# Performance work log

Hardware: AMD Instinct MI355X
Metric: run time of the kernel (lower is better)

Reference implementation:

```python
import jax, jax.numpy as jnp
import numpy as np
import math

MEMORY_SIZE = 50000
FEATURE_SIZE = 4096  # = 64*8*8
HASH_SIZE = 128
B, C, H, W = 64, 64, 8, 8


def setup_inputs() -> dict:
    key = jax.random.key(0)
    k1, k2, k3, k4 = jax.random.split(key, 4)
    stdv = 1.0 / math.sqrt(FEATURE_SIZE)
    feature = jax.random.normal(k1, (B, C, H, W), dtype=jnp.float32)
    memory = jax.random.uniform(k2, (MEMORY_SIZE, FEATURE_SIZE), minval=-stdv, maxval=stdv, dtype=jnp.float32)
    # nn.Linear default init: U(-1/sqrt(fan_in), 1/sqrt(fan_in))
    hash_W = jax.random.uniform(k3, (HASH_SIZE, FEATURE_SIZE), minval=-stdv, maxval=stdv, dtype=jnp.float32)
    hash_b = jax.random.uniform(k4, (HASH_SIZE,), minval=-stdv, maxval=stdv, dtype=jnp.float32)
    return {"feature": feature, "memory": memory, "hash_W": hash_W, "hash_b": hash_b}


def _binarize(x, hash_W, hash_b):
    # 0.5 * (sign(Linear(x) - 0.5) + 1)  -> values in {0, 1} (0.5 only on measure-zero ties)
    return 0.5 * (jnp.sign(x @ hash_W.T + hash_b - 0.5) + 1.0)


def reference(feature, memory, hash_W, hash_b):
    b, c, h, w = feature.shape
    flat = feature.reshape(b, c * h * w)                      # [B, F]
    hm = _binarize(memory, hash_W, hash_b)                    # [M, 128]
    hf = _binarize(flat, hash_W, hash_b)                      # [B, 128]
    # For binary a,b: |a - b| = a + b - 2ab, so the L1 (Hamming) distance is a GEMM:
    HD = (hf.sum(-1, keepdims=True) + hm.sum(-1)[None, :]
          - 2.0 * (hf @ hm.T))                                # [B, M]
    idx = jnp.argmin(HD, axis=1)                              # [B]
    recon = memory[idx]                                       # gather nearest memory rows
    return recon.reshape(b, c, h, w)
```

## Files before the change

kernel.cpp:

```cpp
#include <hip/hip_runtime.h>
#include <hip/hip_bf16.h>
#include <stdint.h>
#include <stddef.h>

typedef __attribute__((ext_vector_type(8))) short s8v;
typedef __attribute__((ext_vector_type(4))) float f32x4;
typedef __attribute__((ext_vector_type(4))) uint32_t u32x4;
typedef __attribute__((ext_vector_type(4))) unsigned short u16x4;

#define KDIM 4096
#define NH   128
#define MMEM 50000
#define BFEAT 64
#define NGRP 3125
#define NBLK 256
#define NGMAX 13
#define NSEG 8

static __device__ __forceinline__ unsigned short f2bf(float f) {
  union { float f; uint32_t u; } c; c.f = f;
  uint32_t u = c.u;
  return (unsigned short)((u + 0x7FFFu + ((u >> 16) & 1u)) >> 16);
}

static __device__ __forceinline__ short f2bfs(float f) {
  __hip_bfloat16 h = __float2bfloat16(f);
  short s;
  __builtin_memcpy(&s, &h, sizeof(s));
  return s;
}

__global__ __launch_bounds__(256) void prep_kernel(
    const float* __restrict__ W, unsigned short* __restrict__ Wb,
    const float* __restrict__ flat, const float* __restrict__ hb,
    unsigned char* __restrict__ hf_bytes, unsigned int* __restrict__ keys) {
  const int bid = blockIdx.x;
  const int t   = threadIdx.x;
  if (bid < 512) {
    if (bid == 0 && t < BFEAT) keys[t] = 0xFFFFFFFFu;
    int i = bid * 256 + t;
    f32x4 v = reinterpret_cast<const f32x4*>(W)[i];
    u16x4 o;
    o[0] = f2bf(v[0]); o[1] = f2bf(v[1]); o[2] = f2bf(v[2]); o[3] = f2bf(v[3]);
    reinterpret_cast<u16x4*>(Wb)[i] = o;
  } else {
    int did  = (bid - 512) * 4 + (t >> 6);
    int n = did & 127, b = did >> 7;
    int lane = t & 63;
    const f32x4* fa = reinterpret_cast<const f32x4*>(flat + (size_t)b * KDIM);
    const f32x4* wa = reinterpret_cast<const f32x4*>(W + (size_t)n * KDIM);
    float s = 0.f;
#pragma unroll 4
    for (int q = 0; q < 16; ++q) {
      f32x4 x = fa[lane + 64 * q], y = wa[lane + 64 * q];
      s += x[0] * y[0] + x[1] * y[1] + x[2] * y[2] + x[3] * y[3];
    }
    for (int o = 32; o; o >>= 1) s += __shfl_down(s, o, 64);
    if (lane == 0) hf_bytes[b * NH + n] = (s + hb[n] - 0.5f) > 0.f ? 1 : 0;
  }
}


__global__ __launch_bounds__(512, 2) void hash_bits_kernel(
    const float* __restrict__ A,
    const unsigned short* __restrict__ Wb,
    const float* __restrict__ hb,
    uint32_t* __restrict__ out_bits) {
  __shared__ short Abuf[2][NGMAX * 16 * 64];
  __shared__ unsigned short smb[NGMAX * 16][8];

  const int t    = threadIdx.x;
  const int lane = t & 63;
  const int w    = t >> 6;
  const int l15  = lane & 15;
  const int kq   = lane >> 4;
  const int b    = blockIdx.x;
  const int koff = b & 63;
  const int g0   = (b * NGRP) >> 8;
  const int NG   = (((b + 1) * NGRP) >> 8) - g0;
  const int row0 = g0 * 16;

  const float* srcA[4];
  int ldsoff[4];
#pragma unroll
  for (int p = 0; p < 4; ++p) {
    int P  = t + 512 * p;
    int g  = P >> 7;
    int q  = P & 127;
    int r  = q >> 3;
    int kg = q & 7;
    srcA[p]   = A + (size_t)(row0 + g * 16 + r) * KDIM + kg * 8;
    ldsoff[p] = (g * 16 + r) * 64 + ((kg ^ (r & 7)) << 3);
  }
  const bool v3 = (t + 1536) < NG * 128;

  const unsigned short* pb = Wb + (size_t)(16 * w + l15) * KDIM + kq * 8;
  const float hbv = hb[16 * w + l15];

  f32x4 acc[NGMAX];
#pragma unroll
  for (int g = 0; g < NGMAX; ++g) acc[g] = (f32x4){0.f, 0.f, 0.f, 0.f};

  f32x4 aR[4][2];
  s8v bA0, bA1, bB0, bB1;

#define PCH(S) (((S) + koff) & 63)

#define LOADA(CH) do {                                                        \
  const f32x4* q0 = reinterpret_cast<const f32x4*>(srcA[0] + (CH) * 64);      \
  aR[0][0] = q0[0]; aR[0][1] = q0[1];                                         \
  const f32x4* q1 = reinterpret_cast<const f32x4*>(srcA[1] + (CH) * 64);      \
  aR[1][0] = q1[0]; aR[1][1] = q1[1];                                         \
  const f32x4* q2 = reinterpret_cast<const f32x4*>(srcA[2] + (CH) * 64);      \
  aR[2][0] = q2[0]; aR[2][1] = q2[1];                                         \
  if (v3) {                                                                   \
    const f32x4* q3 = reinterpret_cast<const f32x4*>(srcA[3] + (CH) * 64);    \
    aR[3][0] = q3[0]; aR[3][1] = q3[1];                                       \
  }                                                                           \
} while (0)

#define CVTW1(P, BUFW) do {                                                   \
  s8v av;                                                                     \
  av[0] = f2bfs(aR[P][0][0]); av[1] = f2bfs(aR[P][0][1]);                     \
  av[2] = f2bfs(aR[P][0][2]); av[3] = f2bfs(aR[P][0][3]);                     \
  av[4] = f2bfs(aR[P][1][0]); av[5] = f2bfs(aR[P][1][1]);                     \
  av[6] = f2bfs(aR[P][1][2]); av[7] = f2bfs(aR[P][1][3]);                     \
  *reinterpret_cast<s8v*>(&(BUFW)[ldsoff[P]]) = av;                           \
} while (0)

#define CVTWRITE(BUFW) do {                                                   \
  CVTW1(0, BUFW); CVTW1(1, BUFW); CVTW1(2, BUFW);                             \
  if (v3) CVTW1(3, BUFW);                                                     \
} while (0)

#define LOADB(CH, B0, B1) do {                                                \
  B0 = *reinterpret_cast<const s8v*>(pb + (CH) * 64);                         \
  B1 = *reinterpret_cast<const s8v*>(pb + (CH) * 64 + 32);                    \
} while (0)

#define COMPUTE(BUFR, B0, B1) do {                                            \
  _Pragma("unroll")                                                           \
  for (int g = 0; g < NGMAX; ++g) {                                           \
    const s8v af = *reinterpret_cast<const s8v*>(                             \
        &(BUFR)[(g * 16 + l15) * 64 + ((kq ^ (l15 & 7)) << 3)]);              \
    acc[g] = __builtin_amdgcn_mfma_f32_16x16x32_bf16(af, B0, acc[g], 0, 0, 0);\
  }                                                                           \
  _Pragma("unroll")                                                           \
  for (int g = 0; g < NGMAX; ++g) {                                           \
    const s8v af = *reinterpret_cast<const s8v*>(                             \
        &(BUFR)[(g * 16 + l15) * 64 + (((4 + kq) ^ (l15 & 7)) << 3)]);        \
    acc[g] = __builtin_amdgcn_mfma_f32_16x16x32_bf16(af, B1, acc[g], 0, 0, 0);\
  }                                                                           \
} while (0)

#define BARRIER() do {                                                        \
  asm volatile("s_waitcnt lgkmcnt(0)" ::: "memory");                          \
  __builtin_amdgcn_s_barrier();                                               \
  __builtin_amdgcn_sched_barrier(0);                                          \
} while (0)

#define STEP(S, BUFR, BUFW, B0, B1) do {                                      \
  BARRIER();                                                                  \
  COMPUTE(BUFR, B0, B1);                                                      \
  if ((S) + 1 < 64) CVTWRITE(BUFW);                                           \
  if ((S) + 2 < 64) { LOADA(PCH((S) + 2)); LOADB(PCH((S) + 2), B0, B1); }     \
} while (0)

  LOADA(PCH(0));
  CVTWRITE(Abuf[0]);
  LOADA(PCH(1));
  LOADB(PCH(0), bA0, bA1);
  LOADB(PCH(1), bB0, bB1);

  for (int s2 = 0; s2 < 64; s2 += 2) {
    STEP(s2 + 0, Abuf[0], Abuf[1], bA0, bA1);
    STEP(s2 + 1, Abuf[1], Abuf[0], bB0, bB1);
  }

#pragma unroll
  for (int g = 0; g < NGMAX; ++g) {
#pragma unroll
    for (int r = 0; r < 4; ++r) {
      uint64_t mask = __ballot(acc[g][r] + hbv - 0.5f > 0.f);
      if (l15 == r)
        smb[g * 16 + (lane >> 4) * 4 + r][w] =
            (unsigned short)((mask >> (16 * (lane >> 4))) & 0xFFFFu);
    }
  }
  __syncthreads();
  const int rows = NG * 16;
  if (t < rows) {
    uint32_t w0 = (uint32_t)smb[t][0] | ((uint32_t)smb[t][1] << 16);
    uint32_t w1 = (uint32_t)smb[t][2] | ((uint32_t)smb[t][3] << 16);
    uint32_t w2 = (uint32_t)smb[t][4] | ((uint32_t)smb[t][5] << 16);
    uint32_t w3 = (uint32_t)smb[t][6] | ((uint32_t)smb[t][7] << 16);
    reinterpret_cast<u32x4*>(out_bits)[row0 + t] = (u32x4){w0, w1, w2, w3};
  }
}

__global__ __launch_bounds__(256) void argmin_part_kernel(
    const uint32_t* __restrict__ hm_bits, const unsigned char* __restrict__ hf_bytes,
    int M, unsigned int* __restrict__ keys) {
  __shared__ uint32_t red[256];
  const int b   = blockIdx.x & (BFEAT - 1);
  const int seg = blockIdx.x / BFEAT;
  const int span = (M + NSEG - 1) / NSEG;
  const int m0 = seg * span;
  int m1 = m0 + span; if (m1 > M) m1 = M;
  const int t = threadIdx.x;
  uint64_t hf0 = 0, hf1 = 0;
  const unsigned char* hfb = hf_bytes + b * NH;
  for (int c = 0; c < 64; ++c) {
    hf0 |= (uint64_t)(hfb[c] & 1u) << c;
    hf1 |= (uint64_t)(hfb[c + 64] & 1u) << c;
  }
  int hfsum = __popcll(hf0) + __popcll(hf1);
  uint32_t best = 0xFFFFFFFFu;
  for (int m = m0 + t; m < m1; m += 256) {
    u32x4 pv = reinterpret_cast<const u32x4*>(hm_bits)[m];
    uint64_t h0 = (uint64_t)pv[0] | ((uint64_t)pv[1] << 32);
    uint64_t h1 = (uint64_t)pv[2] | ((uint64_t)pv[3] << 32);
    int hmsum = __popcll(h0) + __popcll(h1);
    int dot   = __popcll(h0 & hf0) + __popcll(h1 & hf1);
    int hd    = hfsum + hmsum - 2 * dot;
    uint32_t key = ((uint32_t)hd << 16) | (uint32_t)m;
    best = best < key ? best : key;
  }
  red[t] = best;
  __syncthreads();
  for (int s = 128; s > 0; s >>= 1) {
    if (t < s) red[t] = red[t] < red[t + s] ? red[t] : red[t + s];
    __syncthreads();
  }
  if (t == 0) atomicMin(&keys[b], red[0]);
}

__global__ __launch_bounds__(256) void gather_kernel(
    const float* __restrict__ memory, const unsigned int* __restrict__ keys,
    float* __restrict__ out) {
  int b = blockIdx.x;
  int t = threadIdx.x;
  int m = (int)(keys[b] & 0xFFFFu);
  const f32x4* src = reinterpret_cast<const f32x4*>(memory + (size_t)m * KDIM);
  f32x4* dst = reinterpret_cast<f32x4*>(out + (size_t)b * KDIM);
#pragma unroll
  for (int c = 0; c < 4; ++c) dst[t + 256 * c] = src[t + 256 * c];
}

extern "C" void kernel_launch(void* const* d_in, const int* in_sizes, int n_in,
                              void* d_out, int out_size, void* d_ws, size_t ws_size,
                              hipStream_t stream) {
  const float* feature = (const float*)d_in[0];
  const float* memory  = (const float*)d_in[1];
  const float* hash_W  = (const float*)d_in[2];
  const float* hash_b  = (const float*)d_in[3];
  float* out = (float*)d_out;

  char* ws = (char*)d_ws;
  unsigned short* Wb       = (unsigned short*)ws;
  uint32_t*       hm_bits  = (uint32_t*)(ws + 1048576);
  unsigned char*  hf_bytes = (unsigned char*)(ws + 1048576 + 800000);
  unsigned int*   keys     = (unsigned int*)(ws + 1048576 + 800000 + 8192);

  prep_kernel<<<2560, 256, 0, stream>>>(hash_W, Wb, feature, hash_b, hf_bytes, keys);
  hash_bits_kernel<<<NBLK, 512, 0, stream>>>(memory, Wb, hash_b, hm_bits);
  argmin_part_kernel<<<BFEAT * NSEG, 256, 0, stream>>>(hm_bits, hf_bytes, MMEM, keys);
  gather_kernel<<<BFEAT, 256, 0, stream>>>(memory, keys, out);
}
```

Measured before the change: 175.2 us.

## Double hash-bits grid to 512 blocks and fuse argmin with gather

The hash-bits GEMM now runs on 512 blocks with fewer row groups each (NGMAX 7, occupancy hint raised to 4 blocks per CU), so more CUs are busy and register pressure drops. Row indices are clamped so tail blocks cannot read past the memory array. The segmented argmin with atomicMin and the separate gather kernel become one kernel: a 512-thread block per query scans all memory rows and then copies the winning row itself. This removes a launch and the key initialisation, but each query's scan now runs in a single block instead of eight.

```diff
diff --git a/kernel.cpp b/kernel.cpp
--- a/kernel.cpp
+++ b/kernel.cpp
@@ -13,9 +13,9 @@
 #define MMEM 50000
 #define BFEAT 64
 #define NGRP 3125
-#define NBLK 256
-#define NGMAX 13
-#define NSEG 8
+#define NBLK 512
+#define NGMAX 7
+#define MLANES 512
 
 static __device__ __forceinline__ unsigned short f2bf(float f) {
   union { float f; uint32_t u; } c; c.f = f;
@@ -33,11 +33,10 @@
 __global__ __launch_bounds__(256) void prep_kernel(
     const float* __restrict__ W, unsigned short* __restrict__ Wb,
     const float* __restrict__ flat, const float* __restrict__ hb,
-    unsigned char* __restrict__ hf_bytes, unsigned int* __restrict__ keys) {
+    unsigned char* __restrict__ hf_bytes) {
   const int bid = blockIdx.x;
   const int t   = threadIdx.x;
   if (bid < 512) {
-    if (bid == 0 && t < BFEAT) keys[t] = 0xFFFFFFFFu;
     int i = bid * 256 + t;
     f32x4 v = reinterpret_cast<const f32x4*>(W)[i];
     u16x4 o;
@@ -61,7 +60,7 @@
 }
 
 
-__global__ __launch_bounds__(512, 2) void hash_bits_kernel(
+__global__ __launch_bounds__(512, 4) void hash_bits_kernel(
     const float* __restrict__ A,
     const unsigned short* __restrict__ Wb,
     const float* __restrict__ hb,
@@ -76,23 +75,25 @@
   const int kq   = lane >> 4;
   const int b    = blockIdx.x;
   const int koff = b & 63;
-  const int g0   = (b * NGRP) >> 8;
-  const int NG   = (((b + 1) * NGRP) >> 8) - g0;
+  const int g0   = (b * NGRP) >> 9;
+  const int NG   = (((b + 1) * NGRP) >> 9) - g0;
   const int row0 = g0 * 16;
 
-  const float* srcA[4];
-  int ldsoff[4];
-#pragma unroll
-  for (int p = 0; p < 4; ++p) {
+  const float* srcA[2];
+  int ldsoff[2];
+#pragma unroll
+  for (int p = 0; p < 2; ++p) {
     int P  = t + 512 * p;
     int g  = P >> 7;
     int q  = P & 127;
     int r  = q >> 3;
     int kg = q & 7;
-    srcA[p]   = A + (size_t)(row0 + g * 16 + r) * KDIM + kg * 8;
+    int row = row0 + g * 16 + r;
+    if (row > MMEM - 1) row = MMEM - 1;
+    srcA[p]   = A + (size_t)row * KDIM + kg * 8;
     ldsoff[p] = (g * 16 + r) * 64 + ((kg ^ (r & 7)) << 3);
   }
-  const bool v3 = (t + 1536) < NG * 128;
+  const bool v1 = (t + 512) < NG * 128;
 
   const unsigned short* pb = Wb + (size_t)(16 * w + l15) * KDIM + kq * 8;
   const float hbv = hb[16 * w + l15];
@@ -101,7 +102,7 @@
 #pragma unroll
   for (int g = 0; g < NGMAX; ++g) acc[g] = (f32x4){0.f, 0.f, 0.f, 0.f};
 
-  f32x4 aR[4][2];
+  f32x4 aR[2][2];
   s8v bA0, bA1, bB0, bB1;
 
 #define PCH(S) (((S) + koff) & 63)
@@ -109,13 +110,9 @@
 #define LOADA(CH) do {                                                        \
   const f32x4* q0 = reinterpret_cast<const f32x4*>(srcA[0] + (CH) * 64);      \
   aR[0][0] = q0[0]; aR[0][1] = q0[1];                                         \
-  const f32x4* q1 = reinterpret_cast<const f32x4*>(srcA[1] + (CH) * 64);      \
-  aR[1][0] = q1[0]; aR[1][1] = q1[1];                                         \
-  const f32x4* q2 = reinterpret_cast<const f32x4*>(srcA[2] + (CH) * 64);      \
-  aR[2][0] = q2[0]; aR[2][1] = q2[1];                                         \
-  if (v3) {                                                                   \
-    const f32x4* q3 = reinterpret_cast<const f32x4*>(srcA[3] + (CH) * 64);    \
-    aR[3][0] = q3[0]; aR[3][1] = q3[1];                                       \
+  if (v1) {                                                                   \
+    const f32x4* q1 = reinterpret_cast<const f32x4*>(srcA[1] + (CH) * 64);    \
+    aR[1][0] = q1[0]; aR[1][1] = q1[1];                                       \
   }                                                                           \
 } while (0)
 
@@ -129,8 +126,8 @@
 } while (0)
 
 #define CVTWRITE(BUFW) do {                                                   \
-  CVTW1(0, BUFW); CVTW1(1, BUFW); CVTW1(2, BUFW);                             \
-  if (v3) CVTW1(3, BUFW);                                                     \
+  CVTW1(0, BUFW);                                                             \
+  if (v1) CVTW1(1, BUFW);                                                     \
 } while (0)
 
 #define LOADB(CH, B0, B1) do {                                                \
@@ -198,15 +195,11 @@
   }
 }
 
-__global__ __launch_bounds__(256) void argmin_part_kernel(
+__global__ __launch_bounds__(512) void argmin_gather_kernel(
     const uint32_t* __restrict__ hm_bits, const unsigned char* __restrict__ hf_bytes,
-    int M, unsigned int* __restrict__ keys) {
-  __shared__ uint32_t red[256];
-  const int b   = blockIdx.x & (BFEAT - 1);
-  const int seg = blockIdx.x / BFEAT;
-  const int span = (M + NSEG - 1) / NSEG;
-  const int m0 = seg * span;
-  int m1 = m0 + span; if (m1 > M) m1 = M;
+    const float* __restrict__ memory, float* __restrict__ out) {
+  __shared__ uint32_t red[MLANES];
+  const int b = blockIdx.x;
   const int t = threadIdx.x;
   uint64_t hf0 = 0, hf1 = 0;
   const unsigned char* hfb = hf_bytes + b * NH;
@@ -216,7 +209,7 @@
   }
   int hfsum = __popcll(hf0) + __popcll(hf1);
   uint32_t best = 0xFFFFFFFFu;
-  for (int m = m0 + t; m < m1; m += 256) {
+  for (int m = t; m < MMEM; m += MLANES) {
     u32x4 pv = reinterpret_cast<const u32x4*>(hm_bits)[m];
     uint64_t h0 = (uint64_t)pv[0] | ((uint64_t)pv[1] << 32);
     uint64_t h1 = (uint64_t)pv[2] | ((uint64_t)pv[3] << 32);
@@ -228,23 +221,15 @@
   }
   red[t] = best;
   __syncthreads();
-  for (int s = 128; s > 0; s >>= 1) {
+  for (int s = MLANES / 2; s > 0; s >>= 1) {
     if (t < s) red[t] = red[t] < red[t + s] ? red[t] : red[t + s];
     __syncthreads();
   }
-  if (t == 0) atomicMin(&keys[b], red[0]);
-}
-
-__global__ __launch_bounds__(256) void gather_kernel(
-    const float* __restrict__ memory, const unsigned int* __restrict__ keys,
-    float* __restrict__ out) {
-  int b = blockIdx.x;
-  int t = threadIdx.x;
-  int m = (int)(keys[b] & 0xFFFFu);
+  const int m = (int)(red[0] & 0xFFFFu);
   const f32x4* src = reinterpret_cast<const f32x4*>(memory + (size_t)m * KDIM);
   f32x4* dst = reinterpret_cast<f32x4*>(out + (size_t)b * KDIM);
-#pragma unroll
-  for (int c = 0; c < 4; ++c) dst[t + 256 * c] = src[t + 256 * c];
+  dst[t]       = src[t];
+  dst[t + 512] = src[t + 512];
 }
 
 extern "C" void kernel_launch(void* const* d_in, const int* in_sizes, int n_in,
@@ -260,10 +245,8 @@
   unsigned short* Wb       = (unsigned short*)ws;
   uint32_t*       hm_bits  = (uint32_t*)(ws + 1048576);
   unsigned char*  hf_bytes = (unsigned char*)(ws + 1048576 + 800000);
-  unsigned int*   keys     = (unsigned int*)(ws + 1048576 + 800000 + 8192);
-
-  prep_kernel<<<2560, 256, 0, stream>>>(hash_W, Wb, feature, hash_b, hf_bytes, keys);
+
+  prep_kernel<<<2560, 256, 0, stream>>>(hash_W, Wb, feature, hash_b, hf_bytes);
   hash_bits_kernel<<<NBLK, 512, 0, stream>>>(memory, Wb, hash_b, hm_bits);
-  argmin_part_kernel<<<BFEAT * NSEG, 256, 0, stream>>>(hm_bits, hf_bytes, MMEM, keys);
-  gather_kernel<<<BFEAT, 256, 0, stream>>>(memory, keys, out);
-}
+  argmin_gather_kernel<<<BFEAT, 512, 0, stream>>>(hm_bits, hf_bytes, memory, out);
+}
```

Result: slower. 199.6 us (+13.9%).

## Fuse prep, argmin and gather kernels; convert hash weights in-loop

Applied to the files above, without the earlier changes.

Drops the separate prep kernel. The hash weights are now loaded as fp32 and converted to bf16 inside the MFMA loop. The feature hash, the argmin over all memory rows and the gather are merged into one kernel with one block per batch item, so there is no atomic and no key initialisation. This cuts the launch count from four to two and removes intermediate global buffers. In exchange, the hash weight loads are twice as large, the conversions run inside the hot loop, and the argmin now runs on only 64 blocks, each scanning all 50000 rows and recomputing 128 dot products per block.

```diff
diff --git a/kernel.cpp b/kernel.cpp
--- a/kernel.cpp
+++ b/kernel.cpp
@@ -6,7 +6,6 @@
 typedef __attribute__((ext_vector_type(8))) short s8v;
 typedef __attribute__((ext_vector_type(4))) float f32x4;
 typedef __attribute__((ext_vector_type(4))) uint32_t u32x4;
-typedef __attribute__((ext_vector_type(4))) unsigned short u16x4;
 
 #define KDIM 4096
 #define NH   128
@@ -15,13 +14,7 @@
 #define NGRP 3125
 #define NBLK 256
 #define NGMAX 13
-#define NSEG 8
-
-static __device__ __forceinline__ unsigned short f2bf(float f) {
-  union { float f; uint32_t u; } c; c.f = f;
-  uint32_t u = c.u;
-  return (unsigned short)((u + 0x7FFFu + ((u >> 16) & 1u)) >> 16);
-}
+#define MLANES 512
 
 static __device__ __forceinline__ short f2bfs(float f) {
   __hip_bfloat16 h = __float2bfloat16(f);
@@ -30,40 +23,10 @@
   return s;
 }
 
-__global__ __launch_bounds__(256) void prep_kernel(
-    const float* __restrict__ W, unsigned short* __restrict__ Wb,
-    const float* __restrict__ flat, const float* __restrict__ hb,
-    unsigned char* __restrict__ hf_bytes, unsigned int* __restrict__ keys) {
-  const int bid = blockIdx.x;
-  const int t   = threadIdx.x;
-  if (bid < 512) {
-    if (bid == 0 && t < BFEAT) keys[t] = 0xFFFFFFFFu;
-    int i = bid * 256 + t;
-    f32x4 v = reinterpret_cast<const f32x4*>(W)[i];
-    u16x4 o;
-    o[0] = f2bf(v[0]); o[1] = f2bf(v[1]); o[2] = f2bf(v[2]); o[3] = f2bf(v[3]);
-    reinterpret_cast<u16x4*>(Wb)[i] = o;
-  } else {
-    int did  = (bid - 512) * 4 + (t >> 6);
-    int n = did & 127, b = did >> 7;
-    int lane = t & 63;
-    const f32x4* fa = reinterpret_cast<const f32x4*>(flat + (size_t)b * KDIM);
-    const f32x4* wa = reinterpret_cast<const f32x4*>(W + (size_t)n * KDIM);
-    float s = 0.f;
-#pragma unroll 4
-    for (int q = 0; q < 16; ++q) {
-      f32x4 x = fa[lane + 64 * q], y = wa[lane + 64 * q];
-      s += x[0] * y[0] + x[1] * y[1] + x[2] * y[2] + x[3] * y[3];
-    }
-    for (int o = 32; o; o >>= 1) s += __shfl_down(s, o, 64);
-    if (lane == 0) hf_bytes[b * NH + n] = (s + hb[n] - 0.5f) > 0.f ? 1 : 0;
-  }
-}
-
 
 __global__ __launch_bounds__(512, 2) void hash_bits_kernel(
     const float* __restrict__ A,
-    const unsigned short* __restrict__ Wb,
+    const float* __restrict__ Wf,
     const float* __restrict__ hb,
     uint32_t* __restrict__ out_bits) {
   __shared__ short Abuf[2][NGMAX * 16 * 64];
@@ -94,7 +57,7 @@
   }
   const bool v3 = (t + 1536) < NG * 128;
 
-  const unsigned short* pb = Wb + (size_t)(16 * w + l15) * KDIM + kq * 8;
+  const float* pbf = Wf + (size_t)(16 * w + l15) * KDIM + kq * 8;
   const float hbv = hb[16 * w + l15];
 
   f32x4 acc[NGMAX];
@@ -102,7 +65,7 @@
   for (int g = 0; g < NGMAX; ++g) acc[g] = (f32x4){0.f, 0.f, 0.f, 0.f};
 
   f32x4 aR[4][2];
-  s8v bA0, bA1, bB0, bB1;
+  f32x4 bA[4], bB[4];
 
 #define PCH(S) (((S) + koff) & 63)
 
@@ -133,23 +96,34 @@
   if (v3) CVTW1(3, BUFW);                                                     \
 } while (0)
 
-#define LOADB(CH, B0, B1) do {                                                \
-  B0 = *reinterpret_cast<const s8v*>(pb + (CH) * 64);                         \
-  B1 = *reinterpret_cast<const s8v*>(pb + (CH) * 64 + 32);                    \
-} while (0)
-
-#define COMPUTE(BUFR, B0, B1) do {                                            \
+#define LOADB(CH, SET) do {                                                   \
+  const f32x4* qb0 = reinterpret_cast<const f32x4*>(pbf + (CH) * 64);         \
+  SET[0] = qb0[0]; SET[1] = qb0[1];                                           \
+  const f32x4* qb1 = reinterpret_cast<const f32x4*>(pbf + (CH) * 64 + 32);    \
+  SET[2] = qb1[0]; SET[3] = qb1[1];                                           \
+} while (0)
+
+#define COMPUTE(BUFR, SET) do {                                               \
+  s8v b0, b1;                                                                 \
+  b0[0] = f2bfs(SET[0][0]); b0[1] = f2bfs(SET[0][1]);                         \
+  b0[2] = f2bfs(SET[0][2]); b0[3] = f2bfs(SET[0][3]);                         \
+  b0[4] = f2bfs(SET[1][0]); b0[5] = f2bfs(SET[1][1]);                         \
+  b0[6] = f2bfs(SET[1][2]); b0[7] = f2bfs(SET[1][3]);                         \
+  b1[0] = f2bfs(SET[2][0]); b1[1] = f2bfs(SET[2][1]);                         \
+  b1[2] = f2bfs(SET[2][2]); b1[3] = f2bfs(SET[2][3]);                         \
+  b1[4] = f2bfs(SET[3][0]); b1[5] = f2bfs(SET[3][1]);                         \
+  b1[6] = f2bfs(SET[3][2]); b1[7] = f2bfs(SET[3][3]);                         \
   _Pragma("unroll")                                                           \
   for (int g = 0; g < NGMAX; ++g) {                                           \
     const s8v af = *reinterpret_cast<const s8v*>(                             \
         &(BUFR)[(g * 16 + l15) * 64 + ((kq ^ (l15 & 7)) << 3)]);              \
-    acc[g] = __builtin_amdgcn_mfma_f32_16x16x32_bf16(af, B0, acc[g], 0, 0, 0);\
+    acc[g] = __builtin_amdgcn_mfma_f32_16x16x32_bf16(af, b0, acc[g], 0, 0, 0);\
   }                                                                           \
   _Pragma("unroll")                                                           \
   for (int g = 0; g < NGMAX; ++g) {                                           \
     const s8v af = *reinterpret_cast<const s8v*>(                             \
         &(BUFR)[(g * 16 + l15) * 64 + (((4 + kq) ^ (l15 & 7)) << 3)]);        \
-    acc[g] = __builtin_amdgcn_mfma_f32_16x16x32_bf16(af, B1, acc[g], 0, 0, 0);\
+    acc[g] = __builtin_amdgcn_mfma_f32_16x16x32_bf16(af, b1, acc[g], 0, 0, 0);\
   }                                                                           \
 } while (0)
 
@@ -159,22 +133,22 @@
   __builtin_amdgcn_sched_barrier(0);                                          \
 } while (0)
 
-#define STEP(S, BUFR, BUFW, B0, B1) do {                                      \
+#define STEP(S, BUFR, BUFW, SET) do {                                         \
   BARRIER();                                                                  \
-  COMPUTE(BUFR, B0, B1);                                                      \
+  COMPUTE(BUFR, SET);                                                         \
   if ((S) + 1 < 64) CVTWRITE(BUFW);                                           \
-  if ((S) + 2 < 64) { LOADA(PCH((S) + 2)); LOADB(PCH((S) + 2), B0, B1); }     \
+  if ((S) + 2 < 64) { LOADA(PCH((S) + 2)); LOADB(PCH((S) + 2), SET); }        \
 } while (0)
 
   LOADA(PCH(0));
   CVTWRITE(Abuf[0]);
   LOADA(PCH(1));
-  LOADB(PCH(0), bA0, bA1);
-  LOADB(PCH(1), bB0, bB1);
+  LOADB(PCH(0), bA);
+  LOADB(PCH(1), bB);
 
   for (int s2 = 0; s2 < 64; s2 += 2) {
-    STEP(s2 + 0, Abuf[0], Abuf[1], bA0, bA1);
-    STEP(s2 + 1, Abuf[1], Abuf[0], bB0, bB1);
+    STEP(s2 + 0, Abuf[0], Abuf[1], bA);
+    STEP(s2 + 1, Abuf[1], Abuf[0], bB);
   }
 
 #pragma unroll
@@ -198,25 +172,41 @@
   }
 }
 
-__global__ __launch_bounds__(256) void argmin_part_kernel(
-    const uint32_t* __restrict__ hm_bits, const unsigned char* __restrict__ hf_bytes,
-    int M, unsigned int* __restrict__ keys) {
-  __shared__ uint32_t red[256];
-  const int b   = blockIdx.x & (BFEAT - 1);
-  const int seg = blockIdx.x / BFEAT;
-  const int span = (M + NSEG - 1) / NSEG;
-  const int m0 = seg * span;
-  int m1 = m0 + span; if (m1 > M) m1 = M;
-  const int t = threadIdx.x;
+__global__ __launch_bounds__(512) void argmin_gather_kernel(
+    const uint32_t* __restrict__ hm_bits, const float* __restrict__ feature,
+    const float* __restrict__ Wf, const float* __restrict__ hb,
+    const float* __restrict__ memory, float* __restrict__ out) {
+  __shared__ unsigned char hfb[NH];
+  __shared__ uint32_t red[MLANES];
+  const int b    = blockIdx.x;
+  const int t    = threadIdx.x;
+  const int w    = t >> 6;
+  const int lane = t & 63;
+
+  const f32x4* fv = reinterpret_cast<const f32x4*>(feature + (size_t)b * KDIM);
+#pragma unroll 2
+  for (int d = 0; d < 16; ++d) {
+    const int n = w * 16 + d;
+    const f32x4* wv = reinterpret_cast<const f32x4*>(Wf + (size_t)n * KDIM);
+    float s = 0.f;
+#pragma unroll 4
+    for (int q = 0; q < 16; ++q) {
+      f32x4 x = fv[lane + 64 * q], y = wv[lane + 64 * q];
+      s += x[0] * y[0] + x[1] * y[1] + x[2] * y[2] + x[3] * y[3];
+    }
+    for (int o = 32; o; o >>= 1) s += __shfl_down(s, o, 64);
+    if (lane == 0) hfb[n] = (s + hb[n] - 0.5f) > 0.f ? 1 : 0;
+  }
+  __syncthreads();
+
   uint64_t hf0 = 0, hf1 = 0;
-  const unsigned char* hfb = hf_bytes + b * NH;
   for (int c = 0; c < 64; ++c) {
     hf0 |= (uint64_t)(hfb[c] & 1u) << c;
     hf1 |= (uint64_t)(hfb[c + 64] & 1u) << c;
   }
   int hfsum = __popcll(hf0) + __popcll(hf1);
   uint32_t best = 0xFFFFFFFFu;
-  for (int m = m0 + t; m < m1; m += 256) {
+  for (int m = t; m < MMEM; m += MLANES) {
     u32x4 pv = reinterpret_cast<const u32x4*>(hm_bits)[m];
     uint64_t h0 = (uint64_t)pv[0] | ((uint64_t)pv[1] << 32);
     uint64_t h1 = (uint64_t)pv[2] | ((uint64_t)pv[3] << 32);
@@ -228,23 +218,15 @@
   }
   red[t] = best;
   __syncthreads();
-  for (int s = 128; s > 0; s >>= 1) {
+  for (int s = MLANES / 2; s > 0; s >>= 1) {
     if (t < s) red[t] = red[t] < red[t + s] ? red[t] : red[t + s];
     __syncthreads();
   }
-  if (t == 0) atomicMin(&keys[b], red[0]);
-}
-
-__global__ __launch_bounds__(256) void gather_kernel(
-    const float* __restrict__ memory, const unsigned int* __restrict__ keys,
-    float* __restrict__ out) {
-  int b = blockIdx.x;
-  int t = threadIdx.x;
-  int m = (int)(keys[b] & 0xFFFFu);
+  const int m = (int)(red[0] & 0xFFFFu);
   const f32x4* src = reinterpret_cast<const f32x4*>(memory + (size_t)m * KDIM);
   f32x4* dst = reinterpret_cast<f32x4*>(out + (size_t)b * KDIM);
-#pragma unroll
-  for (int c = 0; c < 4; ++c) dst[t + 256 * c] = src[t + 256 * c];
+  dst[t]       = src[t];
+  dst[t + 512] = src[t + 512];
 }
 
 extern "C" void kernel_launch(void* const* d_in, const int* in_sizes, int n_in,
@@ -256,14 +238,9 @@
   const float* hash_b  = (const float*)d_in[3];
   float* out = (float*)d_out;
 
-  char* ws = (char*)d_ws;
-  unsigned short* Wb       = (unsigned short*)ws;
-  uint32_t*       hm_bits  = (uint32_t*)(ws + 1048576);
-  unsigned char*  hf_bytes = (unsigned char*)(ws + 1048576 + 800000);
-  unsigned int*   keys     = (unsigned int*)(ws + 1048576 + 800000 + 8192);
-
-  prep_kernel<<<2560, 256, 0, stream>>>(hash_W, Wb, feature, hash_b, hf_bytes, keys);
-  hash_bits_kernel<<<NBLK, 512, 0, stream>>>(memory, Wb, hash_b, hm_bits);
-  argmin_part_kernel<<<BFEAT * NSEG, 256, 0, stream>>>(hm_bits, hf_bytes, MMEM, keys);
-  gather_kernel<<<BFEAT, 256, 0, stream>>>(memory, keys, out);
-}
+  uint32_t* hm_bits = (uint32_t*)d_ws;
+
+  hash_bits_kernel<<<NBLK, 512, 0, stream>>>(memory, hash_W, hash_b, hm_bits);
+  argmin_gather_kernel<<<BFEAT, 512, 0, stream>>>(hm_bits, feature, hash_W,
+                                                  hash_b, memory, out);
+}
```

After: 213.9 us. 22.1% more time.
